# Optimization experiments

Hardware: AMD Instinct MI355X
Metric: run time of the kernel (lower is better)

Reference implementation:

```python
import jax, jax.numpy as jnp
import numpy as np

# Faithful JAX port of kornia.filters.median_blur as used by MedianBlur in eval mode:
#  - zero padding to keep 'same' spatial size
#  - unfold kxk neighborhoods, take the (k*k)//2-th order statistic (k odd -> exact median,
#    matching torch.median's lower-median convention for odd counts)

def _median_blur(img, k):
    # img: [B, C, H, W]; k: odd python int
    pad = k // 2
    B, C, H, W = img.shape
    x = jnp.pad(img, ((0, 0), (0, 0), (pad, pad), (pad, pad)))  # zero pad (kornia default)
    # Stack the k*k shifted views -> [B, C, k*k, H, W] (fixed small loop over kernel taps)
    patches = jnp.stack(
        [x[:, :, i:i + H, j:j + W] for i in range(k) for j in range(k)], axis=2
    )
    med_idx = (k * k) // 2  # k odd -> unique middle element
    return jnp.sort(patches, axis=2)[:, :, med_idx]


def setup_inputs() -> dict:
    key = jax.random.key(0)
    img = jax.random.normal(key, (8, 3, 512, 512), dtype=jnp.float32)
    return {"img": img, "kernel_size": 5}


def reference(img, kernel_size):
    return _median_blur(img, int(kernel_size))
```

## Files before the change

### kernel.cpp

```cpp
#include <hip/hip_runtime.h>


typedef __fp16 h2 __attribute__((ext_vector_type(2)));

#define MIN2(a, b) __builtin_elementwise_min((a), (b))
#define MAX2(a, b) __builtin_elementwise_max((a), (b))

__device__ __forceinline__ void cswap(h2& a, h2& b) {
    h2 lo = MIN2(a, b);
    h2 hi = MAX2(a, b);
    a = lo; b = hi;
}

#define SORT4 { cswap(v0,v1); cswap(v2,v3); cswap(v0,v2); cswap(v1,v3); cswap(v1,v2); }

#define COL_TOP2(x0,x1,x2,x3,x4,o3,o4) { \
    h2 lo01=MIN2(x0,x1), hi01=MAX2(x0,x1); \
    h2 lo23=MIN2(x2,x3), hi23=MAX2(x2,x3); \
    h2 mx4 = MAX2(hi01,hi23); \
    h2 s4  = MAX2(MIN2(hi01,hi23), MAX2(lo01,lo23)); \
    h2 hi  = MAX2(mx4, x4), lo = MIN2(mx4, x4); \
    (o4) = hi; (o3) = MAX2(s4, lo); }

#define COL_BOT2(x0,x1,x2,x3,x4,o0,o1) { \
    h2 lo01=MIN2(x0,x1), hi01=MAX2(x0,x1); \
    h2 lo23=MIN2(x2,x3), hi23=MAX2(x2,x3); \
    h2 mn4 = MIN2(lo01,lo23); \
    h2 s4  = MIN2(MAX2(lo01,lo23), MIN2(hi01,hi23)); \
    h2 lo  = MIN2(mn4, x4), hi = MAX2(mn4, x4); \
    (o0) = lo; (o1) = MIN2(s4, hi); }

#define COL_TOP3(a0,a1,a2,a3,a4,o2,o3,o4) { \
    h2 v0=a0,v1=a1,v2=a2,v3=a3,v4=a4; SORT4; \
    cswap(v3,v4); cswap(v2,v3); cswap(v1,v2); (o2)=v2; (o3)=v3; (o4)=v4; (void)v0; }

#define COL_MID3(a0,a1,a2,a3,a4,o1,o2,o3) { \
    h2 v0=a0,v1=a1,v2=a2,v3=a3,v4=a4; SORT4; \
    cswap(v3,v4); cswap(v2,v3); cswap(v1,v2); cswap(v0,v1); (o1)=v1; (o2)=v2; (o3)=v3; }

#define COL_BOT3(a0,a1,a2,a3,a4,o0,o1,o2) { \
    h2 v0=a0,v1=a1,v2=a2,v3=a3,v4=a4; SORT4; \
    cswap(v0,v4); cswap(v1,v4); cswap(v2,v4); (o0)=v0; (o1)=v1; (o2)=v2; (void)v3; }

#define MERGE23(a0,a1,p0,p1,p2,L0,L1,L2,L3,L4) { \
    h2 e0 = MIN2(a0,p0), t = MAX2(a0,p0); \
    h2 e1 = MIN2(t,p2),  e2 = MAX2(t,p2); \
    h2 o0 = MIN2(a1,p1), o1 = MAX2(a1,p1); \
    (L0)=e0; (L1)=MIN2(o0,e1); (L2)=MAX2(o0,e1); (L3)=MIN2(o1,e2); (L4)=MAX2(o1,e2); }

__global__ __launch_bounds__(256) void median5_kernel(const float* __restrict__ img,
                                                      float* __restrict__ out)
{
    const int W = 512, H = 512;
    const int t  = blockIdx.x * 64 + threadIdx.x;
    const int x0 = t * 2;
    const int ty = blockIdx.y * 4 + threadIdx.y;
    const int y0 = ty * 8;
    const int p  = blockIdx.z;

    const float* __restrict__ base = img + ((size_t)p << 18);
    float* __restrict__ obase = out + ((size_t)p << 18) + x0;

    const bool okL = (x0 >= 2);
    const bool okR = (x0 + 3 < W);

    h2 r[5][5];

#define LOAD_ROW(yy, SL) do { \
    const int _y = (yy); \
    if ((unsigned)_y < (unsigned)H) { \
        const float* _rp = base + _y * W + x0; \
        float2 l0 = okL ? *(const float2*)(_rp - 2) : make_float2(0.f, 0.f); \
        float2 l1 = *(const float2*)(_rp); \
        float2 l2 = okR ? *(const float2*)(_rp + 2) : make_float2(0.f, 0.f); \
        h2 v0 = __builtin_amdgcn_cvt_pkrtz(l0.x, l0.y); \
        h2 v1 = __builtin_amdgcn_cvt_pkrtz(l0.y, l1.x); \
        h2 v2 = __builtin_amdgcn_cvt_pkrtz(l1.x, l1.y); \
        h2 v3 = __builtin_amdgcn_cvt_pkrtz(l1.y, l2.x); \
        h2 v4 = __builtin_amdgcn_cvt_pkrtz(l2.x, l2.y); \
        SORT4; \
        cswap(v3,v4); cswap(v2,v3); cswap(v1,v2); cswap(v0,v1); \
        r[SL][0]=v0; r[SL][1]=v1; r[SL][2]=v2; r[SL][3]=v3; r[SL][4]=v4; \
    } else { \
        h2 z = {(__fp16)0.f, (__fp16)0.f}; \
        r[SL][0]=z; r[SL][1]=z; r[SL][2]=z; r[SL][3]=z; r[SL][4]=z; \
    } \
} while (0)

    LOAD_ROW(y0 - 2, 0);
    LOAD_ROW(y0 - 1, 1);
    LOAD_ROW(y0 + 0, 2);
    LOAD_ROW(y0 + 1, 3);

#define PROC(i, RA, RB, RC, RD, RE) do { \
    LOAD_ROW(y0 + (i) + 2, RE); \
    h2 a0,a1, p0,p1,p2, mm0,mm1,mm2, q0,q1,q2, d0,d1; \
    COL_TOP2(r[RA][0], r[RB][0], r[RC][0], r[RD][0], r[RE][0], a0, a1); \
    COL_TOP3(r[RA][1], r[RB][1], r[RC][1], r[RD][1], r[RE][1], p0, p1, p2); \
    COL_MID3(r[RA][2], r[RB][2], r[RC][2], r[RD][2], r[RE][2], mm0, mm1, mm2); \
    COL_BOT3(r[RA][3], r[RB][3], r[RC][3], r[RD][3], r[RE][3], q0, q1, q2); \
    COL_BOT2(r[RA][4], r[RB][4], r[RC][4], r[RD][4], r[RE][4], d0, d1); \
    h2 L0,L1,L2,L3,L4, R0,R1,R2,R3,R4; \
    MERGE23(a0, a1, p0, p1, p2, L0, L1, L2, L3, L4); \
    MERGE23(d0, d1, q0, q1, q2, R0, R1, R2, R3, R4); \
     \
    h2 u  = MAX2(L1,R1), v  = MIN2(L3,R3); \
    h2 O1 = MIN2(u,v),   O2 = MAX2(u,v); \
    h2 u2 = MAX2(L0,R0), v2 = MIN2(L4,R4); \
    h2 F1 = MIN2(u2,v2), F2 = MAX2(u2,v2); \
    h2 G0 = MIN2(L2,R2), G1 = MAX2(L2,R2); \
    h2 E2 = MAX2(G0,F1), E3 = MIN2(G1,F2); \
    h2 Sa = MIN2(O1,E2), Sb = MAX2(O1,E2); \
    h2 Sc = MIN2(O2,E3), Sd = MAX2(O2,E3); \
     \
    h2 med = MIN2( MIN2(MAX2(Sa,mm2), MAX2(Sb,mm1)), \
                   MIN2(MAX2(Sc,mm0), Sd) ); \
    float2 o; \
    o.x = (float)med.x; \
    o.y = (float)med.y; \
    *reinterpret_cast<float2*>(obase + (y0 + (i)) * W) = o; \
} while (0)

    PROC(0, 0, 1, 2, 3, 4);
    PROC(1, 1, 2, 3, 4, 0);
    PROC(2, 2, 3, 4, 0, 1);
    PROC(3, 3, 4, 0, 1, 2);
    PROC(4, 4, 0, 1, 2, 3);
    PROC(5, 0, 1, 2, 3, 4);
    PROC(6, 1, 2, 3, 4, 0);
    PROC(7, 2, 3, 4, 0, 1);
}

extern "C" void kernel_launch(void* const* d_in, const int* in_sizes, int n_in,
                              void* d_out, int out_size, void* d_ws, size_t ws_size,
                              hipStream_t stream)
{
    const float* img = (const float*)d_in[0];
    float* out = (float*)d_out;

    dim3 block(64, 4, 1);
    dim3 grid(512 / 2 / 64, 512 / 8 / 4, 24);
    median5_kernel<<<grid, block, 0, stream>>>(img, out);
}
```

Baseline: 87.44 us.

## Share four-row column sorts between adjacent output rows in median filter

Outputs are now computed two rows at a time. The four shared rows of each column window are sorted once, and each output row's fifth element is inserted separately, so the 4-element sorting network is no longer repeated per row. A six-slot row ring buffer replaces the five-slot one, which raises register pressure and may lower occupancy.

```diff
diff --git a/kernel.cpp b/kernel.cpp
--- a/kernel.cpp
+++ b/kernel.cpp
@@ -13,40 +13,33 @@
 }
 
 #define SORT4 { cswap(v0,v1); cswap(v2,v3); cswap(v0,v2); cswap(v1,v3); cswap(v1,v2); }
-
-#define COL_TOP2(x0,x1,x2,x3,x4,o3,o4) { \
-    h2 lo01=MIN2(x0,x1), hi01=MAX2(x0,x1); \
-    h2 lo23=MIN2(x2,x3), hi23=MAX2(x2,x3); \
-    h2 mx4 = MAX2(hi01,hi23); \
-    h2 s4  = MAX2(MIN2(hi01,hi23), MAX2(lo01,lo23)); \
-    h2 hi  = MAX2(mx4, x4), lo = MIN2(mx4, x4); \
-    (o4) = hi; (o3) = MAX2(s4, lo); }
-
-#define COL_BOT2(x0,x1,x2,x3,x4,o0,o1) { \
-    h2 lo01=MIN2(x0,x1), hi01=MAX2(x0,x1); \
-    h2 lo23=MIN2(x2,x3), hi23=MAX2(x2,x3); \
-    h2 mn4 = MIN2(lo01,lo23); \
-    h2 s4  = MIN2(MAX2(lo01,lo23), MIN2(hi01,hi23)); \
-    h2 lo  = MIN2(mn4, x4), hi = MAX2(mn4, x4); \
-    (o0) = lo; (o1) = MIN2(s4, hi); }
-
-#define COL_TOP3(a0,a1,a2,a3,a4,o2,o3,o4) { \
-    h2 v0=a0,v1=a1,v2=a2,v3=a3,v4=a4; SORT4; \
-    cswap(v3,v4); cswap(v2,v3); cswap(v1,v2); (o2)=v2; (o3)=v3; (o4)=v4; (void)v0; }
-
-#define COL_MID3(a0,a1,a2,a3,a4,o1,o2,o3) { \
-    h2 v0=a0,v1=a1,v2=a2,v3=a3,v4=a4; SORT4; \
-    cswap(v3,v4); cswap(v2,v3); cswap(v1,v2); cswap(v0,v1); (o1)=v1; (o2)=v2; (o3)=v3; }
-
-#define COL_BOT3(a0,a1,a2,a3,a4,o0,o1,o2) { \
-    h2 v0=a0,v1=a1,v2=a2,v3=a3,v4=a4; SORT4; \
-    cswap(v0,v4); cswap(v1,v4); cswap(v2,v4); (o0)=v0; (o1)=v1; (o2)=v2; (void)v3; }
+#define CSORT4(a,b,c,d) { cswap(a,b); cswap(c,d); cswap(a,c); cswap(b,d); cswap(b,c); }
 
 #define MERGE23(a0,a1,p0,p1,p2,L0,L1,L2,L3,L4) { \
     h2 e0 = MIN2(a0,p0), t = MAX2(a0,p0); \
     h2 e1 = MIN2(t,p2),  e2 = MAX2(t,p2); \
     h2 o0 = MIN2(a1,p1), o1 = MAX2(a1,p1); \
     (L0)=e0; (L1)=MIN2(o0,e1); (L2)=MAX2(o0,e1); (L3)=MIN2(o1,e2); (L4)=MAX2(o1,e2); }
+
+#define SELECT_STORE(a0,a1,p0,p1,p2,mm0,mm1,mm2,q0,q1,q2,d0,d1, orow) { \
+    h2 L0,L1,L2,L3,L4, R0,R1,R2,R3,R4; \
+    MERGE23(a0, a1, p0, p1, p2, L0, L1, L2, L3, L4); \
+    MERGE23(d0, d1, q0, q1, q2, R0, R1, R2, R3, R4); \
+    h2 u  = MAX2(L1,R1), v  = MIN2(L3,R3); \
+    h2 O1 = MIN2(u,v),   O2 = MAX2(u,v); \
+    h2 u2 = MAX2(L0,R0), v2 = MIN2(L4,R4); \
+    h2 F1 = MIN2(u2,v2), F2 = MAX2(u2,v2); \
+    h2 G0 = MIN2(L2,R2), G1 = MAX2(L2,R2); \
+    h2 E2 = MAX2(G0,F1), E3 = MIN2(G1,F2); \
+    h2 Sa = MIN2(O1,E2), Sb = MAX2(O1,E2); \
+    h2 Sc = MIN2(O2,E3), Sd = MAX2(O2,E3); \
+    h2 med = MIN2( MIN2(MAX2(Sa,mm2), MAX2(Sb,mm1)), \
+                   MIN2(MAX2(Sc,mm0), Sd) ); \
+    float2 o; \
+    o.x = (float)med.x; \
+    o.y = (float)med.y; \
+    *reinterpret_cast<float2*>(obase + (orow) * W) = o; \
+}
 
 __global__ __launch_bounds__(256) void median5_kernel(const float* __restrict__ img,
                                                       float* __restrict__ out)
@@ -64,7 +57,7 @@
     const bool okL = (x0 >= 2);
     const bool okR = (x0 + 3 < W);
 
-    h2 r[5][5];
+    h2 r[6][5];
 
 #define LOAD_ROW(yy, SL) do { \
     const int _y = (yy); \
@@ -87,48 +80,68 @@
     } \
 } while (0)
 
+#define PAIR(i, EA, S1, S2, S3, S4, EB) do { \
+    h2 Aa0,Aa1, Ap0,Ap1,Ap2, Am0,Am1,Am2, Aq0,Aq1,Aq2, Ad0,Ad1; \
+    h2 Ba0,Ba1, Bp0,Bp1,Bp2, Bm0,Bm1,Bm2, Bq0,Bq1,Bq2, Bd0,Bd1; \
+     \
+    { h2 m01=MAX2(r[S1][0],r[S2][0]), n01=MIN2(r[S1][0],r[S2][0]); \
+      h2 m23=MAX2(r[S3][0],r[S4][0]), n23=MIN2(r[S3][0],r[S4][0]); \
+      h2 s3=MAX2(m01,m23); \
+      h2 s2=MAX2(MIN2(m01,m23), MAX2(n01,n23)); \
+      { h2 e=r[EA][0]; Aa1=MAX2(s3,e); Aa0=MAX2(s2,MIN2(s3,e)); } \
+      { h2 e=r[EB][0]; Ba1=MAX2(s3,e); Ba0=MAX2(s2,MIN2(s3,e)); } } \
+     \
+    { h2 s0=r[S1][1], s1=r[S2][1], s2=r[S3][1], s3=r[S4][1]; \
+      CSORT4(s0,s1,s2,s3); \
+      { h2 e=r[EA][1], m=MIN2(s3,e); Ap2=MAX2(s3,e); Ap1=MAX2(s2,m); \
+        m=MIN2(s2,m); Ap0=MAX2(s1,m); } \
+      { h2 e=r[EB][1], m=MIN2(s3,e); Bp2=MAX2(s3,e); Bp1=MAX2(s2,m); \
+        m=MIN2(s2,m); Bp0=MAX2(s1,m); } } \
+     \
+    { h2 s0=r[S1][2], s1=r[S2][2], s2=r[S3][2], s3=r[S4][2]; \
+      CSORT4(s0,s1,s2,s3); \
+      { h2 e=r[EA][2], m=MIN2(s3,e); Am2=MAX2(s2,m); m=MIN2(s2,m); \
+        Am1=MAX2(s1,m); m=MIN2(s1,m); Am0=MAX2(s0,m); } \
+      { h2 e=r[EB][2], m=MIN2(s3,e); Bm2=MAX2(s2,m); m=MIN2(s2,m); \
+        Bm1=MAX2(s1,m); m=MIN2(s1,m); Bm0=MAX2(s0,m); } } \
+     \
+    { h2 s0=r[S1][3], s1=r[S2][3], s2=r[S3][3], s3=r[S4][3]; \
+      CSORT4(s0,s1,s2,s3); \
+      { h2 e=r[EA][3], m=MAX2(s0,e); Aq0=MIN2(s0,e); Aq1=MIN2(s1,m); \
+        m=MAX2(s1,m); Aq2=MIN2(s2,m); } \
+      { h2 e=r[EB][3], m=MAX2(s0,e); Bq0=MIN2(s0,e); Bq1=MIN2(s1,m); \
+        m=MAX2(s1,m); Bq2=MIN2(s2,m); } } \
+     \
+    { h2 m01=MAX2(r[S1][4],r[S2][4]), n01=MIN2(r[S1][4],r[S2][4]); \
+      h2 m23=MAX2(r[S3][4],r[S4][4]), n23=MIN2(r[S3][4],r[S4][4]); \
+      h2 s0=MIN2(n01,n23); \
+      h2 s1=MIN2(MAX2(n01,n23), MIN2(m01,m23)); \
+      { h2 e=r[EA][4]; Ad0=MIN2(s0,e); Ad1=MIN2(s1,MAX2(s0,e)); } \
+      { h2 e=r[EB][4]; Bd0=MIN2(s0,e); Bd1=MIN2(s1,MAX2(s0,e)); } } \
+    SELECT_STORE(Aa0,Aa1,Ap0,Ap1,Ap2,Am0,Am1,Am2,Aq0,Aq1,Aq2,Ad0,Ad1, y0+(i)); \
+    SELECT_STORE(Ba0,Ba1,Bp0,Bp1,Bp2,Bm0,Bm1,Bm2,Bq0,Bq1,Bq2,Bd0,Bd1, y0+(i)+1); \
+} while (0)
+
     LOAD_ROW(y0 - 2, 0);
     LOAD_ROW(y0 - 1, 1);
     LOAD_ROW(y0 + 0, 2);
     LOAD_ROW(y0 + 1, 3);
+    LOAD_ROW(y0 + 2, 4);
+    LOAD_ROW(y0 + 3, 5);
 
-#define PROC(i, RA, RB, RC, RD, RE) do { \
-    LOAD_ROW(y0 + (i) + 2, RE); \
-    h2 a0,a1, p0,p1,p2, mm0,mm1,mm2, q0,q1,q2, d0,d1; \
-    COL_TOP2(r[RA][0], r[RB][0], r[RC][0], r[RD][0], r[RE][0], a0, a1); \
-    COL_TOP3(r[RA][1], r[RB][1], r[RC][1], r[RD][1], r[RE][1], p0, p1, p2); \
-    COL_MID3(r[RA][2], r[RB][2], r[RC][2], r[RD][2], r[RE][2], mm0, mm1, mm2); \
-    COL_BOT3(r[RA][3], r[RB][3], r[RC][3], r[RD][3], r[RE][3], q0, q1, q2); \
-    COL_BOT2(r[RA][4], r[RB][4], r[RC][4], r[RD][4], r[RE][4], d0, d1); \
-    h2 L0,L1,L2,L3,L4, R0,R1,R2,R3,R4; \
-    MERGE23(a0, a1, p0, p1, p2, L0, L1, L2, L3, L4); \
-    MERGE23(d0, d1, q0, q1, q2, R0, R1, R2, R3, R4); \
-     \
-    h2 u  = MAX2(L1,R1), v  = MIN2(L3,R3); \
-    h2 O1 = MIN2(u,v),   O2 = MAX2(u,v); \
-    h2 u2 = MAX2(L0,R0), v2 = MIN2(L4,R4); \
-    h2 F1 = MIN2(u2,v2), F2 = MAX2(u2,v2); \
-    h2 G0 = MIN2(L2,R2), G1 = MAX2(L2,R2); \
-    h2 E2 = MAX2(G0,F1), E3 = MIN2(G1,F2); \
-    h2 Sa = MIN2(O1,E2), Sb = MAX2(O1,E2); \
-    h2 Sc = MIN2(O2,E3), Sd = MAX2(O2,E3); \
-     \
-    h2 med = MIN2( MIN2(MAX2(Sa,mm2), MAX2(Sb,mm1)), \
-                   MIN2(MAX2(Sc,mm0), Sd) ); \
-    float2 o; \
-    o.x = (float)med.x; \
-    o.y = (float)med.y; \
-    *reinterpret_cast<float2*>(obase + (y0 + (i)) * W) = o; \
-} while (0)
+    PAIR(0, 0, 1, 2, 3, 4, 5);
 
-    PROC(0, 0, 1, 2, 3, 4);
-    PROC(1, 1, 2, 3, 4, 0);
-    PROC(2, 2, 3, 4, 0, 1);
-    PROC(3, 3, 4, 0, 1, 2);
-    PROC(4, 4, 0, 1, 2, 3);
-    PROC(5, 0, 1, 2, 3, 4);
-    PROC(6, 1, 2, 3, 4, 0);
-    PROC(7, 2, 3, 4, 0, 1);
+    LOAD_ROW(y0 + 4, 0);
+    LOAD_ROW(y0 + 5, 1);
+    PAIR(2, 2, 3, 4, 5, 0, 1);
+
+    LOAD_ROW(y0 + 6, 2);
+    LOAD_ROW(y0 + 7, 3);
+    PAIR(4, 4, 5, 0, 1, 2, 3);
+
+    LOAD_ROW(y0 + 8, 4);
+    LOAD_ROW(y0 + 9, 5);
+    PAIR(6, 0, 1, 2, 3, 4, 5);
 }
 
 extern "C" void kernel_launch(void* const* d_in, const int* in_sizes, int n_in,
```

Result: no change. 86.72 us (-0.8%).
